# Optimization experiments

Hardware: AMD Instinct MI355X
Metric: run time of the kernel (lower is better)

The kernel has to match this reference:

```python
import jax, jax.numpy as jnp
import numpy as np

# NOTE: submodules (VecLayerNorm, VecLinear, VecActivation, VNAttention,
# VNCrossAttention, VNDynamicGraphAttention) are not in the provided source;
# they are reconstructed per standard Vector-Neuron (VN) equivariant layers.

B, C, NQ, NV, K, HEADS = 2, 128, 2048, 2048, 16, 8
HID = 4 * C
EPS = 1e-6
NS = 0.2  # LeakyReLU(0.2) slope used by VecActivation


def vec_layernorm(x, gamma, beta):
    # x: [B,C,3,N] -- equivariant LN: normalize per-channel vector norms,
    # LayerNorm the norms over the channel dim, rescale directions.
    n = jnp.sqrt(jnp.sum(x * x, axis=2, keepdims=True) + EPS)  # [B,C,1,N]
    mu = jnp.mean(n, axis=1, keepdims=True)
    var = jnp.var(n, axis=1, keepdims=True)
    ln = (n - mu) / jnp.sqrt(var + EPS) * gamma[None, :, None, None] + beta[None, :, None, None]
    return x / (n + EPS) * ln


def vlin(x, W):
    # VecLinear: bias-free linear over channel dim (equivariance). x: [B,C,3,N]
    return jnp.einsum('oc,bctn->botn', W, x)


def vn_attention(xq, xkv, Wq, Wk, Wv, Wo):
    # Global equivariant multi-head attention; scores from 3D-vector inner products.
    Bq, Cc, _, Nq = xq.shape
    Dh = Cc // HEADS
    q = vlin(xq, Wq).reshape(Bq, HEADS, Dh, 3, Nq)
    k = vlin(xkv, Wk).reshape(Bq, HEADS, Dh, 3, -1)
    vv = vlin(xkv, Wv).reshape(Bq, HEADS, Dh, 3, -1)
    s = jnp.einsum('bhdtn,bhdtm->bhnm', q, k) / np.float32(np.sqrt(3 * Dh))
    a = jax.nn.softmax(s, axis=-1)
    o = jnp.einsum('bhnm,bhdtm->bhdtn', a, vv).reshape(Bq, Cc, 3, Nq)
    return vlin(o, Wo)


def graph_attention(xq, xv, idx, We):
    # Local kNN graph attention: gather neighbor features by idx, build edge
    # features concat(v_j - q_i, q_i) -> VecLinear, softmax-weight over k neighbors.
    Bq, Cc, _, Nq = xq.shape
    vt = jnp.transpose(xv, (0, 3, 2, 1))                 # [B,Nv,3,C]
    nbr = jax.vmap(lambda vb, ib: vb[ib])(vt, idx)       # [B,Nq,k,3,C]
    qt = jnp.transpose(xq, (0, 3, 2, 1))                 # [B,Nq,3,C]
    center = qt[:, :, None, :, :]
    edge = jnp.concatenate([nbr - center, jnp.broadcast_to(center, nbr.shape)], axis=-1)  # [B,Nq,k,3,2C]
    feat = jnp.einsum('oc,bnktc->bnkto', We, edge)        # [B,Nq,k,3,C]
    s = jnp.einsum('bntc,bnktc->bnk', qt, nbr) / np.float32(np.sqrt(3 * Cc))
    a = jax.nn.softmax(s, axis=-1)
    out = jnp.einsum('bnk,bnkto->bnto', a, feat)          # [B,Nq,3,C]
    return jnp.transpose(out, (0, 3, 2, 1))               # [B,C,3,Nq]


def vn_leaky(x, D):
    # VN-LeakyReLU: learned direction d = D x; reflect negative half-space.
    d = vlin(x, D)
    dot = jnp.sum(x * d, axis=2, keepdims=True)
    dsq = jnp.sum(d * d, axis=2, keepdims=True)
    xneg = x - (dot / (dsq + EPS)) * d
    return NS * x + (1.0 - NS) * jnp.where(dot >= 0, x, xneg)


def setup_inputs() -> dict:
    key = jax.random.key(0)
    ks = jax.random.split(key, 24)

    def w(k_, o, i):
        return jax.random.normal(k_, (o, i), jnp.float32) / np.float32(np.sqrt(i))

    inp = {
        'q': jax.random.normal(ks[0], (B, C, 3, NQ), jnp.float32),
        'v': jax.random.normal(ks[1], (B, C, 3, NV), jnp.float32),
        'q_pos': jax.random.normal(ks[2], (B, NQ, 3), jnp.float32),
        'v_pos': jax.random.normal(ks[3], (B, NV, 3), jnp.float32),
        'self_attn_idx': jax.random.randint(ks[4], (B, NQ, K), 0, NQ),
        'cross_attn_idx': jax.random.randint(ks[5], (B, NQ, K), 0, NV),
        # VecLayerNorm affine params (norm1, norm2, norm_q, norm_v)
        'g1': jnp.ones((C,), jnp.float32), 'b1': jnp.zeros((C,), jnp.float32),
        'g2': jnp.ones((C,), jnp.float32), 'b2': jnp.zeros((C,), jnp.float32),
        'gq': jnp.ones((C,), jnp.float32), 'bq': jnp.zeros((C,), jnp.float32),
        'gv': jnp.ones((C,), jnp.float32), 'bv': jnp.zeros((C,), jnp.float32),
        # self attention (global VN attn + local graph attn + concat merge)
        'Wq_s': w(ks[6], C, C), 'Wk_s': w(ks[7], C, C), 'Wv_s': w(ks[8], C, C), 'Wo_s': w(ks[9], C, C),
        'We_s': w(ks[10], C, 2 * C), 'Wm_s': w(ks[11], C, 2 * C),
        # cross attention
        'Wq_c': w(ks[12], C, C), 'Wk_c': w(ks[13], C, C), 'Wv_c': w(ks[14], C, C), 'Wo_c': w(ks[15], C, C),
        'We_c': w(ks[16], C, 2 * C), 'Wm_c': w(ks[17], C, 2 * C),
        # MLP: VecLinear(C->4C) -> VN-LeakyReLU -> VecLinear(4C->C)
        'W1': w(ks[18], HID, C), 'Dact': w(ks[19], HID, HID), 'W2': w(ks[20], C, HID),
    }
    return inp


def reference(q, v, q_pos, v_pos, self_attn_idx, cross_attn_idx,
              g1, b1, g2, b2, gq, bq, gv, bv,
              Wq_s, Wk_s, Wv_s, Wo_s, We_s, Wm_s,
              Wq_c, Wk_c, Wv_c, Wo_c, We_c, Wm_c,
              W1, Dact, W2):
    # --- self-attention block (norm1 -> global attn + kNN graph attn -> merge -> residual)
    nx = vec_layernorm(q, g1, b1)
    f1 = vn_attention(nx, nx, Wq_s, Wk_s, Wv_s, Wo_s)
    f2 = graph_attention(nx, nx, self_attn_idx, We_s)
    q = q + vlin(jnp.concatenate([f1, f2], axis=1), Wm_s)
    # --- cross-attention block (norm_q / norm_v -> global cross attn + kNN cross graph attn -> merge -> residual)
    nq = vec_layernorm(q, gq, bq)
    nv = vec_layernorm(v, gv, bv)
    f1 = vn_attention(nq, nv, Wq_c, Wk_c, Wv_c, Wo_c)
    f2 = graph_attention(nq, nv, cross_attn_idx, We_c)
    q = q + vlin(jnp.concatenate([f1, f2], axis=1), Wm_c)
    # --- equivariant MLP (norm2 -> VecLinear -> VN-LeakyReLU -> VecLinear -> residual)
    nx = vec_layernorm(q, g2, b2)
    h = vn_leaky(vlin(nx, W1), Dact)
    q = q + vlin(h, W2)
    return q
```

## Files before the change

kernel.cpp:

```cpp
#include <hip/hip_runtime.h>
#include <math.h>

#define B_    2
#define C_    128
#define N_    2048
#define HID_  512
#define HEADS_ 8
#define EPS_  1e-6f
#define NS_   0.2f
#define KSPLIT 8

typedef __attribute__((ext_vector_type(8))) short short8v;
typedef __attribute__((ext_vector_type(4))) float f32x4;
typedef unsigned short ush;
typedef unsigned int u32;

__device__ inline ush f2bf(float f) {
    unsigned u = __float_as_uint(f);
    u += 0x7FFF + ((u >> 16) & 1);
    return (ush)(u >> 16);
}
__device__ inline float bf2f(ush u) { return __uint_as_float((u32)u << 16); }

__device__ inline u32 splitpack(float x) {
    ush hi = f2bf(x);
    float hf = __uint_as_float((u32)hi << 16);
    ush lo = f2bf(x - hf);
    return ((u32)hi << 16) | (u32)lo;
}

__device__ inline void unpack_hi(const u32* buf, short8v& h0, short8v& h1) {
    ush h[16];
    #pragma unroll
    for (int j = 0; j < 16; ++j) h[j] = (ush)(buf[j] >> 16);
    h0 = *(short8v*)&h[0]; h1 = *(short8v*)&h[8];
}

struct LNArgs {
    const float* x[2]; const float* g[2]; const float* bt[2]; ush* ysp[2];
};
__global__ __launch_bounds__(256) void ln_kernel(LNArgs a)
{
    __shared__ float norms[128][32];
    __shared__ float red1[8][32];
    __shared__ float red2[8][32];
    const int s = blockIdx.z;
    const float* x = a.x[s];
    const float* gma = a.g[s];
    const float* bta = a.bt[s];
    ush* ysp = a.ysp[s];

    const int b  = blockIdx.y;
    const int n0 = blockIdx.x * 32;
    const int nn = threadIdx.x & 31;
    const int cg = threadIdx.x >> 5;

    float s1 = 0.f, s2 = 0.f;
    for (int it = 0; it < 16; ++it) {
        int c = it * 8 + cg;
        size_t base = ((size_t)(b * C_ + c) * 3) * N_ + n0 + nn;
        float x0 = x[base], x1 = x[base + N_], x2 = x[base + 2 * N_];
        float nr = sqrtf(x0 * x0 + x1 * x1 + x2 * x2 + EPS_);
        norms[c][nn] = nr;
        s1 += nr; s2 += nr * nr;
    }
    red1[cg][nn] = s1; red2[cg][nn] = s2;
    __syncthreads();
    float S1 = 0.f, S2 = 0.f;
    #pragma unroll
    for (int g = 0; g < 8; ++g) { S1 += red1[g][nn]; S2 += red2[g][nn]; }
    float mu   = S1 * (1.f / 128.f);
    float var  = S2 * (1.f / 128.f) - mu * mu;
    float rstd = rsqrtf(var + EPS_);

    for (int it = 0; it < 16; ++it) {
        int c = it * 8 + cg;
        float nr = norms[c][nn];
        float ln = (nr - mu) * rstd * gma[c] + bta[c];
        float sc = ln / (nr + EPS_);
        size_t base = ((size_t)(b * C_ + c) * 3) * N_ + n0 + nn;
        ysp[base]          = f2bf(x[base] * sc);
        ysp[base + N_]     = f2bf(x[base + N_] * sc);
        ysp[base + 2 * N_] = f2bf(x[base + 2 * N_] * sc);
    }
}

struct WCArgs { const float* src[15]; u32* dst[15]; int n[15]; float scale[15]; };
__global__ __launch_bounds__(256) void wconv_kernel(WCArgs a)
{
    const int w = blockIdx.y;
    const int i = blockIdx.x * 256 + threadIdx.x;
    if (i < a.n[w]) a.dst[w][i] = splitpack(a.src[w][i] * a.scale[w]);
}

template <int XMODE, int OMODE, bool XBF>
__device__ __forceinline__ void gemm_tile(
    const u32* __restrict__ Wsp, int wstride,
    const void* __restrict__ Xv, int K,
    const float* __restrict__ Z, float* __restrict__ Y,
    ush* __restrict__ Ybf, ush* __restrict__ Ytr,
    int b, int m0, int o0loc, int oglob, int Ostr,
    ush (*Wh)[64], ush (*Xh)[64])
{
    const int M = 3 * N_;
    const int tid = threadIdx.x;
    const int lane = tid & 63, wv = tid >> 6;
    const int col = lane & 15, grp = lane >> 4;
    const int wo = wv >> 1, wm = wv & 1;

    f32x4 acc[2][2];
    #pragma unroll
    for (int i = 0; i < 2; ++i)
        #pragma unroll
        for (int j = 0; j < 2; ++j) { f32x4 z = {0.f,0.f,0.f,0.f}; acc[i][j] = z; }

    for (int kk = 0; kk < K; kk += 64) {
        {
            const int o = tid >> 2, kg = tid & 3;
            const u32* src = Wsp + (size_t)(o0loc + o) * wstride + kk + kg * 16;
            u32 buf[16];
            #pragma unroll
            for (int j = 0; j < 4; ++j) *(uint4*)&buf[j * 4] = *(const uint4*)(src + j * 4);
            const int s0 = ((kg * 2)     ^ (o & 7)) << 3;
            const int s1 = ((kg * 2 + 1) ^ (o & 7)) << 3;
            short8v h0, h1; unpack_hi(buf, h0, h1);
            *(short8v*)&Wh[o][s0] = h0; *(short8v*)&Wh[o][s1] = h1;
        }
        if (XMODE == 0) {
            const int m = lane, kq = wv;
            const int s0 = ((kq * 2)     ^ (m & 7)) << 3;
            const int s1 = ((kq * 2 + 1) ^ (m & 7)) << 3;
            if (XBF) {
                const ush* src = (const ush*)Xv + ((size_t)b * K + kk + kq * 16) * M + m0 + m;
                ush h[16];
                #pragma unroll
                for (int j = 0; j < 16; ++j) h[j] = src[(size_t)j * M];
                *(short8v*)&Xh[m][s0] = *(short8v*)&h[0];
                *(short8v*)&Xh[m][s1] = *(short8v*)&h[8];
            } else {
                const u32* src = (const u32*)Xv + ((size_t)b * K + kk + kq * 16) * M + m0 + m;
                u32 buf[16];
                #pragma unroll
                for (int j = 0; j < 16; ++j) buf[j] = src[(size_t)j * M];
                short8v h0, h1; unpack_hi(buf, h0, h1);
                *(short8v*)&Xh[m][s0] = h0; *(short8v*)&Xh[m][s1] = h1;
            }
        } else {
            const int m = tid >> 2, kg = tid & 3;
            const int mg = m0 + m;
            const int n = mg & (N_ - 1), t = mg >> 11;
            const int s0 = ((kg * 2)     ^ (m & 7)) << 3;
            const int s1 = ((kg * 2 + 1) ^ (m & 7)) << 3;
            const ush* src = (const ush*)Xv + ((size_t)(b * N_ + n) * 3 + t) * K + kk + kg * 16;
            ush h[16];
            *(uint4*)&h[0] = *(const uint4*)(src);
            *(uint4*)&h[8] = *(const uint4*)(src + 8);
            *(short8v*)&Xh[m][s0] = *(short8v*)&h[0];
            *(short8v*)&Xh[m][s1] = *(short8v*)&h[8];
        }
        __syncthreads();
        #pragma unroll
        for (int kc = 0; kc < 2; ++kc) {
            const int sk = ((kc * 4 + grp) ^ (col & 7)) << 3;
            short8v ah0 = *(const short8v*)&Wh[wo * 32 + col][sk];
            short8v ah1 = *(const short8v*)&Wh[wo * 32 + 16 + col][sk];
            short8v xh0 = *(const short8v*)&Xh[wm * 32 + col][sk];
            short8v xh1 = *(const short8v*)&Xh[wm * 32 + 16 + col][sk];
            acc[0][0] = __builtin_amdgcn_mfma_f32_16x16x32_bf16(ah0, xh0, acc[0][0], 0, 0, 0);
            acc[0][1] = __builtin_amdgcn_mfma_f32_16x16x32_bf16(ah0, xh1, acc[0][1], 0, 0, 0);
            acc[1][0] = __builtin_amdgcn_mfma_f32_16x16x32_bf16(ah1, xh0, acc[1][0], 0, 0, 0);
            acc[1][1] = __builtin_amdgcn_mfma_f32_16x16x32_bf16(ah1, xh1, acc[1][1], 0, 0, 0);
        }
        __syncthreads();
    }
    #pragma unroll
    for (int of = 0; of < 2; ++of) {
        #pragma unroll
        for (int r = 0; r < 4; ++r) {
            const int o = oglob + wo * 32 + of * 16 + grp * 4 + r;
            #pragma unroll
            for (int mf = 0; mf < 2; ++mf) {
                const int mloc = m0 + wm * 32 + mf * 16 + col;
                const size_t idx = ((size_t)b * Ostr + o) * M + mloc;
                float v = acc[of][mf][r];
                if (OMODE == 0 || OMODE == 5) {
                    if (Z) v += Z[idx];
                    Y[idx] = v;
                }
                if (OMODE == 3 || OMODE == 5) Ybf[idx] = f2bf(v);
                if (OMODE == 4) {
                    ush bv = f2bf(v);
                    const int t = mloc >> 11, n = mloc & (N_ - 1);
                    const int h = (o >> 4) & 7, cl = o & 15;
                    const int d = cl * 3 + t;
                    if (o >= 256) {
                        const int kt = n >> 6, hh = (n >> 5) & 1, db = d >> 4;
                        const size_t idx2 = ((size_t)(b * 8 + h) * 192
                                           + (kt * 2 + hh) * 3 + db) * 512
                                          + (((n >> 3) & 3) * 16 + (d & 15)) * 8 + (n & 7);
                        Ybf[idx2] = bv;
                    } else {
                        const int isK = (o >> 7) & 1;
                        const int qg = n >> 4, half = d >> 5;
                        const size_t idx2 = ((size_t)(isK * 16 + b * 8 + h) * 256
                                           + qg * 2 + half) * 512
                                          + (((d >> 3) & 3) * 16 + (n & 15)) * 8 + (d & 7);
                        Ytr[idx2] = bv;
                    }
                }
            }
        }
    }
}

template <int XMODE, int OMODE, bool XBF>
__global__ __launch_bounds__(256) void gemm_kernel2(
    const u32* __restrict__ Wsp, int wstride,
    const void* __restrict__ Xv,
    const float* __restrict__ Z,
    float* __restrict__ Y, ush* __restrict__ Ybf,
    int Ostr, int obase, int K)
{
    __shared__ __align__(16) ush Wh[64][64];
    __shared__ __align__(16) ush Xh[64][64];
    gemm_tile<XMODE, OMODE, XBF>(Wsp, wstride, Xv, K, Z, Y, Ybf, nullptr,
                            blockIdx.z, blockIdx.x * 64,
                            blockIdx.y * 64, obase + blockIdx.y * 64, Ostr,
                            Wh, Xh);
}

struct QKVArgs {
    const u32* W0; const u32* W1; const u32* W2;
    const ush* X0; const ush* X1; const ush* X2;
};

__global__ __launch_bounds__(256) void qkv_tr_kernel(QKVArgs A,
        ush* __restrict__ vfm, ush* __restrict__ qktb,
        const ush* __restrict__ ts0, ush* __restrict__ td0,
        const ush* __restrict__ ts1, ush* __restrict__ td1)
{
    __shared__ __align__(16) ush Wh[64][64];
    __shared__ __align__(16) ush Xh[64][64];
    __shared__ ush ttile[32][34];
    const int bx = blockIdx.x;
    if (bx < 1152) {
        const int z = bx / 576, rem = bx % 576;
        const int y = rem / 96, x = rem % 96;
        const int wi = y >> 1;
        const u32* W = wi == 0 ? A.W0 : (wi == 1 ? A.W1 : A.W2);
        const ush* X = wi == 0 ? A.X0 : (wi == 1 ? A.X1 : A.X2);
        gemm_tile<0, 4, true>(W, 128, X, 128, nullptr, nullptr, vfm, qktb,
                        z, x * 64, (y & 1) * 64, y * 64, 384,
                        Wh, Xh);
    } else {
        int i = bx - 1152;
        const int which = i / 1536; i %= 1536;
        const ush* src = which ? ts1 : ts0;
        ush* dst = which ? td1 : td0;
        const int x = i & 63, y = (i >> 6) & 3, z = i >> 8;
        const int b = z / 3, t = z % 3;
        const int n0 = x * 32, c0 = y * 32;
        const int tx = threadIdx.x & 31, ty = threadIdx.x >> 5;
        #pragma unroll
        for (int p = 0; p < 4; ++p) {
            int c = c0 + ty + p * 8;
            ttile[ty + p * 8][tx] = src[((size_t)(b * C_ + c) * 3 + t) * N_ + n0 + tx];
        }
        __syncthreads();
        #pragma unroll
        for (int p = 0; p < 4; ++p) {
            int n = n0 + ty + p * 8;
            dst[((size_t)(b * N_ + n) * 3 + t) * C_ + c0 + tx] = ttile[tx][ty + p * 8];
        }
    }
}

__global__ __launch_bounds__(256) void wowe_kernel(
    const u32* __restrict__ Wo, const ush* __restrict__ ao,
    const u32* __restrict__ We, const ush* __restrict__ gb,
    ush* __restrict__ f12)
{
    __shared__ __align__(16) ush Wh[64][64];
    __shared__ __align__(16) ush Xh[64][64];
    const int y = blockIdx.y;
    if (y < 2)
        gemm_tile<0, 3, true>(Wo, 128, ao, 128, nullptr, nullptr, f12, nullptr,
                        blockIdx.z, blockIdx.x * 64, y * 64, y * 64, 256,
                        Wh, Xh);
    else
        gemm_tile<1, 3, true>(We, 256, gb, 256, nullptr, nullptr, f12, nullptr,
                        blockIdx.z, blockIdx.x * 64, (y - 2) * 64, 128 + (y - 2) * 64, 256,
                        Wh, Xh);
}

__global__ __launch_bounds__(256) void attn_mfma_kernel(
    const ush* __restrict__ vfm, const ush* __restrict__ qktb,
    ush* __restrict__ pacc, float* __restrict__ pml)
{
    __shared__ __align__(16) ush Pl[4][2][16][64];

    const int flat = blockIdx.x;
    const int xcd  = flat & 7;
    const int slot = flat >> 3;
    const int gid  = xcd * 4 + (slot >> 6);
    const int q32  = slot & 63;
    const int bh   = gid & 15;
    const int zz   = gid >> 4;

    const int tid = threadIdx.x;
    const int lane = tid & 63, wv = tid >> 6;
    const int col = lane & 15, grp = lane >> 4;
    const int c7  = col & 7;
    const int kz  = zz * 4 + wv;
    const int ks0 = kz * (N_ / KSPLIT);

    const ush* Qpl = qktb + (size_t)bh * 131072;
    const ush* Kpl = qktb + (size_t)(16 + bh) * 131072;
    const ush* Vpl = vfm  + (size_t)bh * 98304;

    short8v qf[2][2];
    #pragma unroll
    for (int qi = 0; qi < 2; ++qi) {
        const int qg = q32 * 2 + qi;
        qf[qi][0] = *(const short8v*)(Qpl + ((size_t)qg * 2 + 0) * 512 + lane * 8);
        qf[qi][1] = *(const short8v*)(Qpl + ((size_t)qg * 2 + 1) * 512 + lane * 8);
    }

    f32x4 acc[2][3];
    #pragma unroll
    for (int qi = 0; qi < 2; ++qi)
        #pragma unroll
        for (int db = 0; db < 3; ++db) { f32x4 z = {0.f,0.f,0.f,0.f}; acc[qi][db] = z; }
    float m_i[2] = {0.f, 0.f};
    float l_l[2] = {0.f, 0.f};

    const int NT = (N_ / KSPLIT) / 64;
    for (int mt = 0; mt < NT; ++mt) {
        const int m0 = ks0 + mt * 64;

        short8v ka[4][2];
        #pragma unroll
        for (int kb = 0; kb < 4; ++kb) {
            const size_t kg = (m0 >> 4) + kb;
            ka[kb][0] = *(const short8v*)(Kpl + (kg * 2 + 0) * 512 + lane * 8);
            ka[kb][1] = *(const short8v*)(Kpl + (kg * 2 + 1) * 512 + lane * 8);
        }
        const int kt = m0 >> 6;
        short8v vf[2][3];
        #pragma unroll
        for (int hh = 0; hh < 2; ++hh)
            #pragma unroll
            for (int db = 0; db < 3; ++db)
                vf[hh][db] = *(const short8v*)(Vpl + (size_t)((kt * 2 + hh) * 3 + db) * 512 + lane * 8);

        f32x4 sf[2][4];
        __builtin_amdgcn_s_setprio(1);
        #pragma unroll
        for (int qi = 0; qi < 2; ++qi)
            #pragma unroll
            for (int kb = 0; kb < 4; ++kb) {
                f32x4 z = {0.f, 0.f, 0.f, 0.f};
                z = __builtin_amdgcn_mfma_f32_16x16x32_bf16(ka[kb][0], qf[qi][0], z, 0, 0, 0);
                z = __builtin_amdgcn_mfma_f32_16x16x32_bf16(ka[kb][1], qf[qi][1], z, 0, 0, 0);
                sf[qi][kb] = z;
            }
        __builtin_amdgcn_s_setprio(0);

        #pragma unroll
        for (int qi = 0; qi < 2; ++qi) {
            float psum = 0.f;
            #pragma unroll
            for (int kb = 0; kb < 4; ++kb) {
                float e0 = __expf(sf[qi][kb][0] - m_i[qi]);
                float e1 = __expf(sf[qi][kb][1] - m_i[qi]);
                float e2 = __expf(sf[qi][kb][2] - m_i[qi]);
                float e3 = __expf(sf[qi][kb][3] - m_i[qi]);
                psum += (e0 + e1) + (e2 + e3);
                u32 r0, r1;
                asm("v_cvt_pk_bf16_f32 %0, %1, %2" : "=v"(r0) : "v"(e0), "v"(e1));
                asm("v_cvt_pk_bf16_f32 %0, %1, %2" : "=v"(r1) : "v"(e2), "v"(e3));
                const int un = (4 * kb + grp) ^ (c7 << 1);
                uint2 pk2; pk2.x = r0; pk2.y = r1;
                *(uint2*)&Pl[wv][qi][col][un << 2] = pk2;
            }
            l_l[qi] += psum;
        }

        __builtin_amdgcn_s_setprio(1);
        #pragma unroll
        for (int qi = 0; qi < 2; ++qi)
            #pragma unroll
            for (int hh = 0; hh < 2; ++hh) {
                const int ur = (8 * hh + 2 * grp) ^ (c7 << 1);
                short8v pf = *(const short8v*)&Pl[wv][qi][col][ur << 2];
                #pragma unroll
                for (int db = 0; db < 3; ++db)
                    acc[qi][db] = __builtin_amdgcn_mfma_f32_16x16x32_bf16(vf[hh][db], pf, acc[qi][db], 0, 0, 0);
            }
        __builtin_amdgcn_s_setprio(0);

        #pragma unroll
        for (int qi = 0; qi < 2; ++qi) {
            float pmax = -1e30f;
            #pragma unroll
            for (int kb = 0; kb < 4; ++kb)
                #pragma unroll
                for (int r = 0; r < 4; ++r) pmax = fmaxf(pmax, sf[qi][kb][r]);
            pmax = fmaxf(pmax, __shfl_xor(pmax, 16, 64));
            pmax = fmaxf(pmax, __shfl_xor(pmax, 32, 64));
            if (!__all(pmax - m_i[qi] <= 8.0f)) {
                float mnew = fmaxf(m_i[qi], pmax);
                float sc = __expf(m_i[qi] - mnew);
                l_l[qi] *= sc;
                #pragma unroll
                for (int db = 0; db < 3; ++db) {
                    acc[qi][db][0] *= sc; acc[qi][db][1] *= sc;
                    acc[qi][db][2] *= sc; acc[qi][db][3] *= sc;
                }
                m_i[qi] = mnew;
            }
        }
    }

    const int ntile = q32 >> 1, qh = q32 & 1;
    const size_t pb = (size_t)(kz * 16 + bh) * 32 + ntile;
    #pragma unroll
    for (int qi = 0; qi < 2; ++qi) {
        float l = l_l[qi];
        l += __shfl_xor(l, 16, 64);
        l += __shfl_xor(l, 32, 64);
        const int q = qh * 32 + qi * 16 + col;
        #pragma unroll
        for (int db = 0; db < 3; ++db)
            #pragma unroll
            for (int r = 0; r < 4; ++r) {
                int d = db * 16 + grp * 4 + r;
                pacc[pb * 3072 + d * 64 + q] = f2bf(acc[qi][db][r]);
            }
        if (grp == 0) {
            pml[pb * 128 + q]      = m_i[qi];
            pml[pb * 128 + 64 + q] = l;
        }
    }
}

__global__ __launch_bounds__(256) void graph_kernel(
    const ush* __restrict__ tq, const ush* __restrict__ tv,
    const int* __restrict__ idx, ush* __restrict__ gbuf)
{
    __shared__ float centerf[384];
    __shared__ ush nbr_l[16][384];
    __shared__ float sd[16];
    __shared__ int nbr_i[16];
    const int b = blockIdx.y, n = blockIdx.x;
    const int tid = threadIdx.x;
    const ush* qrow = tq + (size_t)(b * N_ + n) * 384;
    for (int e = tid; e < 384; e += 256) centerf[e] = bf2f(qrow[e]);
    if (tid < 16) nbr_i[tid] = idx[(size_t)(b * N_ + n) * 16 + tid];
    __syncthreads();

    const int lane = tid & 63, wv = tid >> 6;
    for (int kk = 0; kk < 4; ++kk) {
        int k = wv * 4 + kk;
        const u32* vrow = (const u32*)(tv + ((size_t)b * N_ + nbr_i[k]) * 384);
        float p = 0.f;
        #pragma unroll
        for (int jj = 0; jj < 3; ++jj) {
            int e2 = lane + jj * 64;
            u32 v2 = vrow[e2];
            ((u32*)nbr_l[k])[e2] = v2;
            p += centerf[e2 * 2]     * bf2f((ush)(v2 & 0xffff))
               + centerf[e2 * 2 + 1] * bf2f((ush)(v2 >> 16));
        }
        #pragma unroll
        for (int off = 32; off; off >>= 1) p += __shfl_down(p, off, 64);
        if (lane == 0) sd[k] = p * 0.05103103630798288f;
    }
    __syncthreads();

    float mx = -1e30f;
    #pragma unroll
    for (int k = 0; k < 16; ++k) mx = fmaxf(mx, sd[k]);
    float a[16]; float ssum = 0.f;
    #pragma unroll
    for (int k = 0; k < 16; ++k) { a[k] = __expf(sd[k] - mx); ssum += a[k]; }
    float inv = 1.f / ssum;

    for (int e = tid; e < 384; e += 256) {
        float accv = 0.f;
        #pragma unroll
        for (int k = 0; k < 16; ++k)
            accv += a[k] * bf2f(nbr_l[k][e]);
        accv *= inv;
        float ce = centerf[e];
        int t = e >> 7, c = e & 127;
        size_t gb = ((size_t)(b * N_ + n) * 3 + t) * 256;
        gbuf[gb + c]       = f2bf(accv - ce);
        gbuf[gb + 128 + c] = f2bf(ce);
    }
}

__global__ __launch_bounds__(256) void attn_reduce_kernel(
    const ush* __restrict__ pacc, const float* __restrict__ pml,
    ush* __restrict__ ao)
{
    const int nt = blockIdx.x, bh = blockIdx.y;
    const int b = bh >> 3, h = bh & 7;
    const int tid = threadIdx.x;
    const int q = tid & 63, dg = tid >> 6;

    size_t pb[KSPLIT];
    float m[KSPLIT], l[KSPLIT];
    #pragma unroll
    for (int kz = 0; kz < KSPLIT; ++kz) {
        pb[kz] = (size_t)(kz * 16 + bh) * 32 + nt;
        m[kz] = pml[pb[kz] * 128 + q];
        l[kz] = pml[pb[kz] * 128 + 64 + q];
    }
    float ms = -1e30f;
    #pragma unroll
    for (int kz = 0; kz < KSPLIT; ++kz) ms = fmaxf(ms, m[kz]);
    float w[KSPLIT], ls = 0.f;
    #pragma unroll
    for (int kz = 0; kz < KSPLIT; ++kz) { w[kz] = __expf(m[kz] - ms); ls += l[kz] * w[kz]; }
    const float inv = 1.f / ls;

    const size_t hb = ((size_t)(b * C_ + h * 16)) * 3 * N_;
    #pragma unroll
    for (int j = 0; j < 12; ++j) {
        int d = dg * 12 + j;
        float o = 0.f;
        #pragma unroll
        for (int kz = 0; kz < KSPLIT; ++kz)
            o += bf2f(pacc[pb[kz] * 3072 + d * 64 + q]) * w[kz];
        ao[hb + (size_t)d * N_ + nt * 64 + q] = f2bf(o * inv);
    }
}

__global__ __launch_bounds__(256) void leaky_kernel(const float* __restrict__ x,
                                                    const float* __restrict__ d,
                                                    ush* __restrict__ y)
{
    size_t p = (size_t)blockIdx.x * 256 + threadIdx.x;
    size_t bh = p / N_, n = p % N_;
    size_t base = bh * 3 * N_ + n;
    float x0 = x[base], x1 = x[base + N_], x2 = x[base + 2 * N_];
    float d0 = d[base], d1 = d[base + N_], d2 = d[base + 2 * N_];
    float dot = x0 * d0 + x1 * d1 + x2 * d2;
    float dsq = d0 * d0 + d1 * d1 + d2 * d2;
    float f = dot / (dsq + EPS_);
    bool pos = dot >= 0.f;
    float y0 = pos ? x0 : x0 - f * d0;
    float y1 = pos ? x1 : x1 - f * d1;
    float y2 = pos ? x2 : x2 - f * d2;
    y[base]          = f2bf(NS_ * x0 + (1.f - NS_) * y0);
    y[base + N_]     = f2bf(NS_ * x1 + (1.f - NS_) * y1);
    y[base + 2 * N_] = f2bf(NS_ * x2 + (1.f - NS_) * y2);
}

extern "C" void kernel_launch(void* const* d_in, const int* in_sizes, int n_in,
                              void* d_out, int out_size, void* d_ws, size_t ws_size,
                              hipStream_t stream)
{
    const float* q_in = (const float*)d_in[0];
    const float* v_in = (const float*)d_in[1];
    const int*   idx_s = (const int*)d_in[4];
    const int*   idx_c = (const int*)d_in[5];
    const float* g1 = (const float*)d_in[6];
    const float* b1 = (const float*)d_in[7];
    const float* g2 = (const float*)d_in[8];
    const float* b2 = (const float*)d_in[9];
    const float* gq = (const float*)d_in[10];
    const float* bq = (const float*)d_in[11];
    const float* gv = (const float*)d_in[12];
    const float* bv = (const float*)d_in[13];
    float* out = (float*)d_out;
    float* ws  = (float*)d_ws;

    const size_t S1 = (size_t)B_ * C_ * 3 * N_;
    ush*   nx_b  = (ush*)(ws + 2*S1);
    ush*   nv_b  = (ush*)(ws + 3*S1);
    ush*   vfm   = (ush*)(ws + 4*S1);
    ush*   qktb  = (ush*)(ws + 5*S1) + S1;
    ush*   ao_b  = (ush*)(ws + 7*S1);
    ush*   f12_b = (ush*)(ws + 8*S1);
    float* qa    = ws + 12*S1;
    float* qb    = ws + 13*S1;
    ush*   gbuf_b= (ush*)(ws + 13*S1);
    ush*   t1_b  = (ush*)(ws + 14*S1);
    ush*   t2_b  = (ush*)(ws + 15*S1);
    u32*   wsp   = (u32*)(ws + 16*S1);
    ush*   pacc  = (ush*)(ws + 8*S1);
    float* pml   = (float*)(ws + 2*S1);
    float* hd    = ws;
    float* h1    = ws + 4*S1;
    ush*   h1_b  = (ush*)(ws + 14*S1);
    ush*   h1_b2 = (ush*)(ws + 8*S1);

    const int wn[15]  = {16384,16384,16384,16384,32768,32768,
                         16384,16384,16384,16384,32768,32768,
                         65536,262144,65536};
    u32* wd[15];
    {
        int off = 0;
        for (int i = 0; i < 15; ++i) { wd[i] = wsp + off; off += wn[i]; }
    }
    u32 *Wq_s = wd[0], *Wk_s = wd[1], *Wv_s = wd[2], *Wo_s = wd[3], *We_s = wd[4], *Wm_s = wd[5];
    u32 *Wq_c = wd[6], *Wk_c = wd[7], *Wv_c = wd[8], *Wo_c = wd[9], *We_c = wd[10], *Wm_c = wd[11];
    u32 *W1 = wd[12], *Dact = wd[13], *W2 = wd[14];

    hipMemsetAsync(qktb, 0, (size_t)32 * 131072 * sizeof(ush), stream);

    {
        WCArgs a;
        for (int i = 0; i < 15; ++i) {
            a.src[i] = (const float*)d_in[14 + i];
            a.dst[i] = wd[i];
            a.n[i]   = wn[i];
            a.scale[i] = 1.f;
        }
        a.scale[0] = 0.14433756729740643f;
        a.scale[6] = 0.14433756729740643f;
        wconv_kernel<<<dim3(1024, 15), 256, 0, stream>>>(a);
    }

    dim3 gar(N_ / 64, B_ * HEADS_);
    dim3 ggr(N_, B_);
    dim3 gwe(96, 4, B_);
    dim3 gg128(96, 2, B_);
    dim3 gg512(96, 8, B_);

    {
        LNArgs la{};
        la.x[0] = q_in; la.g[0] = g1; la.bt[0] = b1; la.ysp[0] = nx_b;
        ln_kernel<<<dim3(64, B_, 1), 256, 0, stream>>>(la);
    }
    {
        QKVArgs A{Wq_s, Wk_s, Wv_s, nx_b, nx_b, nx_b};
        qkv_tr_kernel<<<dim3(1152 + 1536), 256, 0, stream>>>(A, vfm, qktb, nx_b, t1_b, nullptr, nullptr);
    }
    attn_mfma_kernel<<<dim3(2048), 256, 0, stream>>>(vfm, qktb, pacc, pml);
    attn_reduce_kernel<<<gar, 256, 0, stream>>>(pacc, pml, ao_b);
    graph_kernel<<<ggr, 256, 0, stream>>>(t1_b, t1_b, idx_s, gbuf_b);
    wowe_kernel<<<gwe, 256, 0, stream>>>(Wo_s, ao_b, We_s, gbuf_b, f12_b);
    gemm_kernel2<0,0,true><<<gg128, 256, 0, stream>>>(Wm_s, 256, f12_b, q_in, qa, nullptr, 128, 0, 256);

    {
        LNArgs la{};
        la.x[0] = qa;   la.g[0] = gq; la.bt[0] = bq; la.ysp[0] = nx_b;
        la.x[1] = v_in; la.g[1] = gv; la.bt[1] = bv; la.ysp[1] = nv_b;
        ln_kernel<<<dim3(64, B_, 2), 256, 0, stream>>>(la);
    }
    {
        QKVArgs A{Wq_c, Wk_c, Wv_c, nx_b, nv_b, nv_b};
        qkv_tr_kernel<<<dim3(1152 + 3072), 256, 0, stream>>>(A, vfm, qktb, nx_b, t1_b, nv_b, t2_b);
    }
    attn_mfma_kernel<<<dim3(2048), 256, 0, stream>>>(vfm, qktb, pacc, pml);
    attn_reduce_kernel<<<gar, 256, 0, stream>>>(pacc, pml, ao_b);
    graph_kernel<<<ggr, 256, 0, stream>>>(t1_b, t2_b, idx_c, gbuf_b);
    wowe_kernel<<<gwe, 256, 0, stream>>>(Wo_c, ao_b, We_c, gbuf_b, f12_b);
    gemm_kernel2<0,0,true><<<gg128, 256, 0, stream>>>(Wm_c, 256, f12_b, qa, qb, nullptr, 128, 0, 256);

    {
        LNArgs la{};
        la.x[0] = qb; la.g[0] = g2; la.bt[0] = b2; la.ysp[0] = nx_b;
        ln_kernel<<<dim3(64, B_, 1), 256, 0, stream>>>(la);
    }
    gemm_kernel2<0,5,true><<<gg512, 256, 0, stream>>>(W1, 128, nx_b, nullptr, h1, h1_b, 512, 0, 128);
    gemm_kernel2<0,0,true><<<gg512, 256, 0, stream>>>(Dact, 512, h1_b, nullptr, hd, nullptr, 512, 0, 512);
    leaky_kernel<<<dim3((B_ * HID_ * N_) / 256), 256, 0, stream>>>(h1, hd, h1_b2);
    gemm_kernel2<0,0,true><<<gg128, 256, 0, stream>>>(W2, 512, h1_b2, qb, out, nullptr, 128, 0, 512);
}
```

Baseline: 263.9 us.

## Fold Wo and We into merge weight, replacing two GEMM stages with one

Because the output projection Wo, the edge projection We and the merge Wm are all bias-free linear maps, Wm·[Wo·ao; We·gb] is rewritten as (Wm_a·Wo)·ao + (Wm_b·We)·gb. The fused weights are built once per call by a small fp32 kernel, and a new wm2 kernel computes both products into one accumulator and adds the residual. This drops the intermediate f12 buffer and one kernel launch per attention block. The per-call weight-product kernel adds some work, and the weights are now multiplied in fp32 before bf16 conversion, which slightly changes rounding.

```diff
diff --git a/kernel.cpp b/kernel.cpp
--- a/kernel.cpp
+++ b/kernel.cpp
@@ -85,12 +85,43 @@
     }
 }
 
-struct WCArgs { const float* src[15]; u32* dst[15]; int n[15]; float scale[15]; };
+struct WCArgs { const float* src[9]; u32* dst[9]; int n[9]; float scale[9]; };
 __global__ __launch_bounds__(256) void wconv_kernel(WCArgs a)
 {
     const int w = blockIdx.y;
     const int i = blockIdx.x * 256 + threadIdx.x;
     if (i < a.n[w]) a.dst[w][i] = splitpack(a.src[w][i] * a.scale[w]);
+}
+
+struct WFArgs {
+    const float* Wm[2]; const float* Wo[2]; const float* We[2];
+    u32* Wfa[2]; u32* Wfb[2];
+};
+__global__ __launch_bounds__(256) void wfuse_kernel(WFArgs a)
+{
+    const int tg = blockIdx.x * 256 + threadIdx.x;
+    const int p = tg / 49152;
+    const int rem = tg % 49152;
+    if (rem < 16384) {
+        const int o = rem >> 7, k = rem & 127;
+        const float* Wm = a.Wm[p];
+        const float* Wo = a.Wo[p];
+        float acc = 0.f;
+        #pragma unroll 4
+        for (int c = 0; c < 128; ++c)
+            acc += Wm[o * 256 + c] * Wo[c * 128 + k];
+        a.Wfa[p][o * 128 + k] = splitpack(acc);
+    } else {
+        const int r2 = rem - 16384;
+        const int o = r2 >> 8, k = r2 & 255;
+        const float* Wm = a.Wm[p];
+        const float* We = a.We[p];
+        float acc = 0.f;
+        #pragma unroll 4
+        for (int c = 0; c < 128; ++c)
+            acc += Wm[o * 256 + 128 + c] * We[c * 256 + k];
+        a.Wfb[p][o * 256 + k] = splitpack(acc);
+    }
 }
 
 template <int XMODE, int OMODE, bool XBF>
@@ -229,6 +260,123 @@
                             Wh, Xh);
 }
 
+__global__ __launch_bounds__(256) void wm2_kernel(
+    const u32* __restrict__ Wfa, const u32* __restrict__ Wfb,
+    const ush* __restrict__ ao, const ush* __restrict__ gb,
+    const float* __restrict__ Z, float* __restrict__ Y)
+{
+    __shared__ __align__(16) ush Wh[64][64];
+    __shared__ __align__(16) ush Xh[64][64];
+    const int M = 3 * N_;
+    const int b = blockIdx.z;
+    const int m0 = blockIdx.x * 64;
+    const int o0 = blockIdx.y * 64;
+    const int tid = threadIdx.x;
+    const int lane = tid & 63, wv = tid >> 6;
+    const int col = lane & 15, grp = lane >> 4;
+    const int wo = wv >> 1, wm = wv & 1;
+
+    f32x4 acc[2][2];
+    #pragma unroll
+    for (int i = 0; i < 2; ++i)
+        #pragma unroll
+        for (int j = 0; j < 2; ++j) { f32x4 z = {0.f,0.f,0.f,0.f}; acc[i][j] = z; }
+
+    for (int kk = 0; kk < 128; kk += 64) {
+        {
+            const int o = tid >> 2, kg = tid & 3;
+            const u32* src = Wfa + (size_t)(o0 + o) * 128 + kk + kg * 16;
+            u32 buf[16];
+            #pragma unroll
+            for (int j = 0; j < 4; ++j) *(uint4*)&buf[j * 4] = *(const uint4*)(src + j * 4);
+            const int s0 = ((kg * 2)     ^ (o & 7)) << 3;
+            const int s1 = ((kg * 2 + 1) ^ (o & 7)) << 3;
+            short8v h0, h1; unpack_hi(buf, h0, h1);
+            *(short8v*)&Wh[o][s0] = h0; *(short8v*)&Wh[o][s1] = h1;
+        }
+        {
+            const int m = lane, kq = wv;
+            const int s0 = ((kq * 2)     ^ (m & 7)) << 3;
+            const int s1 = ((kq * 2 + 1) ^ (m & 7)) << 3;
+            const ush* src = ao + ((size_t)b * 128 + kk + kq * 16) * M + m0 + m;
+            ush h[16];
+            #pragma unroll
+            for (int j = 0; j < 16; ++j) h[j] = src[(size_t)j * M];
+            *(short8v*)&Xh[m][s0] = *(short8v*)&h[0];
+            *(short8v*)&Xh[m][s1] = *(short8v*)&h[8];
+        }
+        __syncthreads();
+        #pragma unroll
+        for (int kc = 0; kc < 2; ++kc) {
+            const int sk = ((kc * 4 + grp) ^ (col & 7)) << 3;
+            short8v ah0 = *(const short8v*)&Wh[wo * 32 + col][sk];
+            short8v ah1 = *(const short8v*)&Wh[wo * 32 + 16 + col][sk];
+            short8v xh0 = *(const short8v*)&Xh[wm * 32 + col][sk];
+            short8v xh1 = *(const short8v*)&Xh[wm * 32 + 16 + col][sk];
+            acc[0][0] = __builtin_amdgcn_mfma_f32_16x16x32_bf16(ah0, xh0, acc[0][0], 0, 0, 0);
+            acc[0][1] = __builtin_amdgcn_mfma_f32_16x16x32_bf16(ah0, xh1, acc[0][1], 0, 0, 0);
+            acc[1][0] = __builtin_amdgcn_mfma_f32_16x16x32_bf16(ah1, xh0, acc[1][0], 0, 0, 0);
+            acc[1][1] = __builtin_amdgcn_mfma_f32_16x16x32_bf16(ah1, xh1, acc[1][1], 0, 0, 0);
+        }
+        __syncthreads();
+    }
+
+    for (int kk = 0; kk < 256; kk += 64) {
+        {
+            const int o = tid >> 2, kg = tid & 3;
+            const u32* src = Wfb + (size_t)(o0 + o) * 256 + kk + kg * 16;
+            u32 buf[16];
+            #pragma unroll
+            for (int j = 0; j < 4; ++j) *(uint4*)&buf[j * 4] = *(const uint4*)(src + j * 4);
+            const int s0 = ((kg * 2)     ^ (o & 7)) << 3;
+            const int s1 = ((kg * 2 + 1) ^ (o & 7)) << 3;
+            short8v h0, h1; unpack_hi(buf, h0, h1);
+            *(short8v*)&Wh[o][s0] = h0; *(short8v*)&Wh[o][s1] = h1;
+        }
+        {
+            const int m = tid >> 2, kg = tid & 3;
+            const int mg = m0 + m;
+            const int n = mg & (N_ - 1), t = mg >> 11;
+            const int s0 = ((kg * 2)     ^ (m & 7)) << 3;
+            const int s1 = ((kg * 2 + 1) ^ (m & 7)) << 3;
+            const ush* src = gb + ((size_t)(b * N_ + n) * 3 + t) * 256 + kk + kg * 16;
+            ush h[16];
+            *(uint4*)&h[0] = *(const uint4*)(src);
+            *(uint4*)&h[8] = *(const uint4*)(src + 8);
+            *(short8v*)&Xh[m][s0] = *(short8v*)&h[0];
+            *(short8v*)&Xh[m][s1] = *(short8v*)&h[8];
+        }
+        __syncthreads();
+        #pragma unroll
+        for (int kc = 0; kc < 2; ++kc) {
+            const int sk = ((kc * 4 + grp) ^ (col & 7)) << 3;
+            short8v ah0 = *(const short8v*)&Wh[wo * 32 + col][sk];
+            short8v ah1 = *(const short8v*)&Wh[wo * 32 + 16 + col][sk];
+            short8v xh0 = *(const short8v*)&Xh[wm * 32 + col][sk];
+            short8v xh1 = *(const short8v*)&Xh[wm * 32 + 16 + col][sk];
+            acc[0][0] = __builtin_amdgcn_mfma_f32_16x16x32_bf16(ah0, xh0, acc[0][0], 0, 0, 0);
+            acc[0][1] = __builtin_amdgcn_mfma_f32_16x16x32_bf16(ah0, xh1, acc[0][1], 0, 0, 0);
+            acc[1][0] = __builtin_amdgcn_mfma_f32_16x16x32_bf16(ah1, xh0, acc[1][0], 0, 0, 0);
+            acc[1][1] = __builtin_amdgcn_mfma_f32_16x16x32_bf16(ah1, xh1, acc[1][1], 0, 0, 0);
+        }
+        __syncthreads();
+    }
+
+    #pragma unroll
+    for (int of = 0; of < 2; ++of) {
+        #pragma unroll
+        for (int r = 0; r < 4; ++r) {
+            const int o = o0 + wo * 32 + of * 16 + grp * 4 + r;
+            #pragma unroll
+            for (int mf = 0; mf < 2; ++mf) {
+                const int mloc = m0 + wm * 32 + mf * 16 + col;
+                const size_t idx = ((size_t)b * 128 + o) * M + mloc;
+                Y[idx] = acc[of][mf][r] + Z[idx];
+            }
+        }
+    }
+}
+
 struct QKVArgs {
     const u32* W0; const u32* W1; const u32* W2;
     const ush* X0; const ush* X1; const ush* X2;
@@ -275,24 +423,6 @@
     }
 }
 
-__global__ __launch_bounds__(256) void wowe_kernel(
-    const u32* __restrict__ Wo, const ush* __restrict__ ao,
-    const u32* __restrict__ We, const ush* __restrict__ gb,
-    ush* __restrict__ f12)
-{
-    __shared__ __align__(16) ush Wh[64][64];
-    __shared__ __align__(16) ush Xh[64][64];
-    const int y = blockIdx.y;
-    if (y < 2)
-        gemm_tile<0, 3, true>(Wo, 128, ao, 128, nullptr, nullptr, f12, nullptr,
-                        blockIdx.z, blockIdx.x * 64, y * 64, y * 64, 256,
-                        Wh, Xh);
-    else
-        gemm_tile<1, 3, true>(We, 256, gb, 256, nullptr, nullptr, f12, nullptr,
-                        blockIdx.z, blockIdx.x * 64, (y - 2) * 64, 128 + (y - 2) * 64, 256,
-                        Wh, Xh);
-}
-
 __global__ __launch_bounds__(256) void attn_mfma_kernel(
     const ush* __restrict__ vfm, const ush* __restrict__ qktb,
     ush* __restrict__ pacc, float* __restrict__ pml)
@@ -583,10 +713,9 @@
     ush*   vfm   = (ush*)(ws + 4*S1);
     ush*   qktb  = (ush*)(ws + 5*S1) + S1;
     ush*   ao_b  = (ush*)(ws + 7*S1);
-    ush*   f12_b = (ush*)(ws + 8*S1);
+    ush*   gbuf_b= (ush*)(ws + 8*S1);
     float* qa    = ws + 12*S1;
     float* qb    = ws + 13*S1;
-    ush*   gbuf_b= (ush*)(ws + 13*S1);
     ush*   t1_b  = (ush*)(ws + 14*S1);
     ush*   t2_b  = (ush*)(ws + 15*S1);
     u32*   wsp   = (u32*)(ws + 16*S1);
@@ -597,37 +726,47 @@
     ush*   h1_b  = (ush*)(ws + 14*S1);
     ush*   h1_b2 = (ush*)(ws + 8*S1);
 
-    const int wn[15]  = {16384,16384,16384,16384,32768,32768,
-                         16384,16384,16384,16384,32768,32768,
-                         65536,262144,65536};
-    u32* wd[15];
+    const int wn[9]   = {16384,16384,16384, 16384,16384,16384, 65536,262144,65536};
+    const int wsrc[9] = {14,15,16, 20,21,22, 26,27,28};
+    u32* wd[9];
     {
         int off = 0;
-        for (int i = 0; i < 15; ++i) { wd[i] = wsp + off; off += wn[i]; }
-    }
-    u32 *Wq_s = wd[0], *Wk_s = wd[1], *Wv_s = wd[2], *Wo_s = wd[3], *We_s = wd[4], *Wm_s = wd[5];
-    u32 *Wq_c = wd[6], *Wk_c = wd[7], *Wv_c = wd[8], *Wo_c = wd[9], *We_c = wd[10], *Wm_c = wd[11];
-    u32 *W1 = wd[12], *Dact = wd[13], *W2 = wd[14];
+        for (int i = 0; i < 9; ++i) { wd[i] = wsp + off; off += wn[i]; }
+    }
+    u32 *Wq_s = wd[0], *Wk_s = wd[1], *Wv_s = wd[2];
+    u32 *Wq_c = wd[3], *Wk_c = wd[4], *Wv_c = wd[5];
+    u32 *W1 = wd[6], *Dact = wd[7], *W2 = wd[8];
+    u32* Wfa_s = wsp + 491520;
+    u32* Wfb_s = Wfa_s + 16384;
+    u32* Wfa_c = Wfb_s + 32768;
+    u32* Wfb_c = Wfa_c + 16384;
 
     hipMemsetAsync(qktb, 0, (size_t)32 * 131072 * sizeof(ush), stream);
 
     {
         WCArgs a;
-        for (int i = 0; i < 15; ++i) {
-            a.src[i] = (const float*)d_in[14 + i];
+        for (int i = 0; i < 9; ++i) {
+            a.src[i] = (const float*)d_in[wsrc[i]];
             a.dst[i] = wd[i];
             a.n[i]   = wn[i];
             a.scale[i] = 1.f;
         }
         a.scale[0] = 0.14433756729740643f;
-        a.scale[6] = 0.14433756729740643f;
-        wconv_kernel<<<dim3(1024, 15), 256, 0, stream>>>(a);
+        a.scale[3] = 0.14433756729740643f;
+        wconv_kernel<<<dim3(1024, 9), 256, 0, stream>>>(a);
+    }
+    {
+        WFArgs a;
+        a.Wm[0] = (const float*)d_in[19]; a.Wo[0] = (const float*)d_in[17]; a.We[0] = (const float*)d_in[18];
+        a.Wm[1] = (const float*)d_in[25]; a.Wo[1] = (const float*)d_in[23]; a.We[1] = (const float*)d_in[24];
+        a.Wfa[0] = Wfa_s; a.Wfb[0] = Wfb_s;
+        a.Wfa[1] = Wfa_c; a.Wfb[1] = Wfb_c;
+        wfuse_kernel<<<dim3(384), 256, 0, stream>>>(a);
     }
 
     dim3 gar(N_ / 64, B_ * HEADS_);
     dim3 ggr(N_, B_);
-    dim3 gwe(96, 4, B_);
-    dim3 gg128(96, 2, B_);
+    dim3 gwm(96, 2, B_);
     dim3 gg512(96, 8, B_);
 
     {
@@ -642,8 +781,7 @@
     attn_mfma_kernel<<<dim3(2048), 256, 0, stream>>>(vfm, qktb, pacc, pml);
     attn_reduce_kernel<<<gar, 256, 0, stream>>>(pacc, pml, ao_b);
     graph_kernel<<<ggr, 256, 0, stream>>>(t1_b, t1_b, idx_s, gbuf_b);
-    wowe_kernel<<<gwe, 256, 0, stream>>>(Wo_s, ao_b, We_s, gbuf_b, f12_b);
-    gemm_kernel2<0,0,true><<<gg128, 256, 0, stream>>>(Wm_s, 256, f12_b, q_in, qa, nullptr, 128, 0, 256);
+    wm2_kernel<<<gwm, 256, 0, stream>>>(Wfa_s, Wfb_s, ao_b, gbuf_b, q_in, qa);
 
     {
         LNArgs la{};
@@ -658,8 +796,7 @@
     attn_mfma_kernel<<<dim3(2048), 256, 0, stream>>>(vfm, qktb, pacc, pml);
     attn_reduce_kernel<<<gar, 256, 0, stream>>>(pacc, pml, ao_b);
     graph_kernel<<<ggr, 256, 0, stream>>>(t1_b, t2_b, idx_c, gbuf_b);
-    wowe_kernel<<<gwe, 256, 0, stream>>>(Wo_c, ao_b, We_c, gbuf_b, f12_b);
-    gemm_kernel2<0,0,true><<<gg128, 256, 0, stream>>>(Wm_c, 256, f12_b, qa, qb, nullptr, 128, 0, 256);
+    wm2_kernel<<<gwm, 256, 0, stream>>>(Wfa_c, Wfb_c, ao_b, gbuf_b, qa, qb);
 
     {
         LNArgs la{};
@@ -669,5 +806,5 @@
     gemm_kernel2<0,5,true><<<gg512, 256, 0, stream>>>(W1, 128, nx_b, nullptr, h1, h1_b, 512, 0, 128);
     gemm_kernel2<0,0,true><<<gg512, 256, 0, stream>>>(Dact, 512, h1_b, nullptr, hd, nullptr, 512, 0, 512);
     leaky_kernel<<<dim3((B_ * HID_ * N_) / 256), 256, 0, stream>>>(h1, hd, h1_b2);
-    gemm_kernel2<0,0,true><<<gg128, 256, 0, stream>>>(W2, 512, h1_b2, qb, out, nullptr, 128, 0, 512);
-}
+    gemm_kernel2<0,0,true><<<dim3(96, 2, B_), 256, 0, stream>>>(W2, 512, h1_b2, qb, out, nullptr, 128, 0, 512);
+}
```

Result: faster. 251.6 us (-4.6%).
